# Performance work log

Hardware: AMD Instinct MI355X
Metric: run time of the kernel (lower is better)

## Reference

```python
import jax, jax.numpy as jnp
from jax import lax
import numpy as np

K, O, I, KS = 4, 128, 128, 5
B, H, W = 32, 64, 64
PAD = 2


def setup_inputs() -> dict:
    key = jax.random.key(0)
    ks = jax.random.split(key, 7)
    x = jax.random.normal(ks[0], (B, I, H, W), dtype=jnp.float32)
    weight = jax.random.normal(ks[1], (K, O, I, KS, KS), dtype=jnp.float32)  # matches torch.randn init
    bias = jax.random.normal(ks[2], (K, O), dtype=jnp.float32)
    # attention: 1x1 convs on a (B,C,1,1) pooled tensor == dense layers
    a1_w = jax.random.normal(ks[3], (I, I), dtype=jnp.float32) * (1.0 / np.sqrt(I))
    a1_b = jax.random.normal(ks[4], (I,), dtype=jnp.float32) * 0.01
    a2_w = jax.random.normal(ks[5], (K, I), dtype=jnp.float32) * (1.0 / np.sqrt(I))
    a2_b = jax.random.normal(ks[6], (K,), dtype=jnp.float32) * 0.01
    return {"x": x, "weight": weight, "bias": bias,
            "a1_w": a1_w, "a1_b": a1_b, "a2_w": a2_w, "a2_b": a2_b}


def reference(x, weight, bias, a1_w, a1_b, a2_w, a2_b):
    Bn = x.shape[0]
    Kn, On, In, kh, kw = weight.shape
    # attention branch: global avg pool -> 1x1 conv -> relu -> 1x1 conv -> softmax over K
    pooled = jnp.mean(x, axis=(2, 3))                       # (B, C)
    h = jax.nn.relu(pooled @ a1_w.T + a1_b)                 # (B, C)
    attn = jax.nn.softmax(h @ a2_w.T + a2_b, axis=1)        # (B, K)
    # K parallel convs fused as one conv with K*O output channels (same math)
    w = weight.reshape(Kn * On, In, kh, kw)
    out = lax.conv_general_dilated(
        x, w, window_strides=(1, 1), padding=((PAD, PAD), (PAD, PAD)),
        dimension_numbers=("NCHW", "OIHW", "NCHW"))        # (B, K*O, H, W)
    Ho, Wo = out.shape[2], out.shape[3]
    out = out.reshape(Bn, Kn, On, Ho, Wo) + bias[None, :, :, None, None]
    # per-sample softmax-weighted combination over the K branches
    return jnp.einsum("bk,bkohw->bohw", attn, out)
```

## Files before the change

kernel.cpp:

```cpp
#include <hip/hip_runtime.h>
#include <stdint.h>

#define BATCH 32
#define ICH 128
#define OCH 128
#define KBR 4
#define HH 64
#define WW 64
#define TAPS 25
#define XROWS 8
#define XCOLS 68
#define XCP 40
#define WROWP 40

typedef __bf16 bf16x8 __attribute__((ext_vector_type(8)));
typedef float f32x4 __attribute__((ext_vector_type(4)));

static __device__ __forceinline__ ushort f2bf(float f) {
    union { float f; uint32_t u; } v; v.f = f;
    uint32_t u = v.u;
    uint32_t r = (u + 0x7FFFu + ((u >> 16) & 1u)) >> 16;
    return (ushort)r;
}
static __device__ __forceinline__ float bf2f(ushort s) {
    union { uint32_t u; float f; } v; v.u = ((uint32_t)s) << 16;
    return v.f;
}

__global__ __launch_bounds__(256) void k_prep(const float* __restrict__ x,
                                              ushort* __restrict__ xT,
                                              float* __restrict__ partial) {
    int blk = blockIdx.x;
    int b = blk >> 6, y = blk & 63;
    __shared__ __align__(16) ushort tile[64][130];
    const float* src = x + ((size_t)b * ICH) * (HH * WW) + (size_t)y * WW;
    int tid = threadIdx.x;
#pragma unroll
    for (int j = 0; j < 8; ++j) {
        int e = (tid + 256 * j) * 4;
        int i = e >> 6, xc = e & 63;
        float4 v = *(const float4*)(src + (size_t)i * (HH * WW) + xc);
        tile[xc + 0][i] = f2bf(v.x);
        tile[xc + 1][i] = f2bf(v.y);
        tile[xc + 2][i] = f2bf(v.z);
        tile[xc + 3][i] = f2bf(v.w);
    }
    __syncthreads();
    uint* dst = (uint*)(xT + (((size_t)b * HH + y) * WW) * ICH);
#pragma unroll
    for (int j = 0; j < 16; ++j) {
        int p = tid + 256 * j;
        int xc = p >> 6, ih = (p & 63) * 2;
        uint v = (uint)tile[xc][ih] | ((uint)tile[xc][ih + 1] << 16);
        dst[p] = v;
    }
    if (tid < 128) {
        float s = 0.f;
        for (int xc = 0; xc < 64; ++xc) s += bf2f(tile[xc][tid]);
        partial[((size_t)b * HH + y) * ICH + tid] = s;
    }
}

__global__ __launch_bounds__(128) void k_attn(const float* __restrict__ partial,
                                              const float* __restrict__ a1_w,
                                              const float* __restrict__ a1_b,
                                              const float* __restrict__ a2_w,
                                              const float* __restrict__ a2_b,
                                              const float* __restrict__ bias,
                                              float* __restrict__ attn,
                                              float* __restrict__ bias_eff) {
    int b = blockIdx.x;
    int t = threadIdx.x;
    __shared__ float pl[128], hh[128], lg[4], at[4];
    {
        float s = 0.f;
        const float* p = partial + (size_t)b * 64 * 128 + t;
        for (int y = 0; y < 64; ++y) s += p[y * 128];
        pl[t] = s * (1.f / 4096.f);
    }
    __syncthreads();
    {
        float a = a1_b[t];
        const float* w1 = a1_w + t * 128;
        for (int i = 0; i < 128; ++i) a += pl[i] * w1[i];
        hh[t] = a > 0.f ? a : 0.f;
    }
    __syncthreads();
    if (t < 4) {
        float l = a2_b[t];
        const float* w2 = a2_w + t * 128;
        for (int i = 0; i < 128; ++i) l += hh[i] * w2[i];
        lg[t] = l;
    }
    __syncthreads();
    if (t == 0) {
        float m = fmaxf(fmaxf(lg[0], lg[1]), fmaxf(lg[2], lg[3]));
        float e0 = expf(lg[0] - m), e1 = expf(lg[1] - m);
        float e2 = expf(lg[2] - m), e3 = expf(lg[3] - m);
        float inv = 1.f / (e0 + e1 + e2 + e3);
        at[0] = e0 * inv; at[1] = e1 * inv; at[2] = e2 * inv; at[3] = e3 * inv;
        attn[b * 4 + 0] = at[0]; attn[b * 4 + 1] = at[1];
        attn[b * 4 + 2] = at[2]; attn[b * 4 + 3] = at[3];
    }
    __syncthreads();
    bias_eff[b * 128 + t] = at[0] * bias[0 * 128 + t] + at[1] * bias[1 * 128 + t] +
                            at[2] * bias[2 * 128 + t] + at[3] * bias[3 * 128 + t];
}

__global__ __launch_bounds__(256) void k_wcomb(const float* __restrict__ weight,
                                               const float* __restrict__ attn,
                                               ushort* __restrict__ Weff) {
    int blk = blockIdx.x;
    int b = blk >> 7, o = blk & 127;
    float a0 = attn[b * 4 + 0], a1 = attn[b * 4 + 1];
    float a2 = attn[b * 4 + 2], a3 = attn[b * 4 + 3];
    __shared__ float wt[3200];
    const float* w = weight + (size_t)o * 3200;
    for (int e = threadIdx.x; e < 3200; e += 256) {
        wt[e] = a0 * w[e] + a1 * w[409600 + e] + a2 * w[819200 + e] + a3 * w[1228800 + e];
    }
    __syncthreads();
    ushort* dst = Weff + ((size_t)(b * 128 + o)) * 3200;
    for (int f = threadIdx.x; f < 3200; f += 256) {
        int t = f >> 7, i = f & 127;
        dst[f] = f2bf(wt[i * 25 + t]);
    }
}

__global__ __launch_bounds__(512) void k_conv(const ushort* __restrict__ xT,
                                              const ushort* __restrict__ Weff,
                                              const float* __restrict__ bias_eff,
                                              float* __restrict__ out) {
    __shared__ __align__(16) ushort lx[XROWS * XCOLS * XCP];
    __shared__ __align__(16) ushort lw[2][128 * WROWP];

    int blk = blockIdx.x;
    int xcd = blk & 7, slot = blk >> 3;
    int b = xcd * 4 + (slot >> 4);
    int rg = slot & 15;
    int y0 = rg * 4;
    int tid = threadIdx.x;
    int lane = tid & 63, wid = tid >> 6;
    int wm = wid >> 2, wn = wid & 3;
    int row16 = lane & 15, kg = lane >> 4;

    f32x4 acc[4][4];
    f32x4 zero = {0.f, 0.f, 0.f, 0.f};
#pragma unroll
    for (int m = 0; m < 4; ++m)
#pragma unroll
        for (int n = 0; n < 4; ++n) acc[m][n] = zero;

    const ushort* xb = xT + ((size_t)b * HH * WW) * ICH;
    const ushort* wb = Weff + ((size_t)b * OCH) * 3200;

    int wo = tid >> 2, wpart = tid & 3;

    {
        for (int q = tid; q < XROWS * XCOLS * 4; q += 512) {
            int s = q / (XCOLS * 4);
            int rem = q - s * (XCOLS * 4);
            int c = rem >> 2, part = rem & 3;
            int gy = y0 - 2 + s, gx = c - 2;
            uint4 val = make_uint4(0u, 0u, 0u, 0u);
            if (gy >= 0 && gy < 64 && gx >= 0 && gx < 64)
                val = *(const uint4*)(xb + ((size_t)(gy * 64 + gx)) * ICH + 0 + part * 8);
            *(uint4*)(&lx[(s * XCOLS + c) * XCP + part * 8]) = val;
        }
        uint4 wv = *(const uint4*)(wb + ((size_t)wo * 25 + 0) * 128 + 0 + wpart * 8);
        *(uint4*)(&lw[0][wo * WROWP + wpart * 8]) = wv;
    }
    __syncthreads();

    for (int g = 0; g < 100; ++g) {
        int buf = g & 1;
        int t = g % 25;
        uint4 wv;
        bool have_next = (g + 1 < 100);
        if (have_next) {
            int gn = g + 1;
            int icn = (gn / 25) * 32, tn = gn % 25;
            wv = *(const uint4*)(wb + ((size_t)wo * 25 + tn) * 128 + icn + wpart * 8);
        }
        {
            int kh = t / 5, kw = t - kh * 5;
            bf16x8 af[4], bfr[4];
#pragma unroll
            for (int m = 0; m < 4; ++m) {
                int o = wm * 64 + m * 16 + row16;
                af[m] = *(const bf16x8*)(&lw[buf][o * WROWP + kg * 8]);
            }
#pragma unroll
            for (int n = 0; n < 4; ++n) {
                int px = wn * 64 + n * 16 + row16;
                int yl = px >> 6, xc = px & 63;
                int s = yl + kh, cc = xc + kw;
                bfr[n] = *(const bf16x8*)(&lx[(s * XCOLS + cc) * XCP + kg * 8]);
            }
#pragma unroll
            for (int m = 0; m < 4; ++m)
#pragma unroll
                for (int n = 0; n < 4; ++n)
                    acc[m][n] = __builtin_amdgcn_mfma_f32_16x16x32_bf16(af[m], bfr[n], acc[m][n], 0, 0, 0);
        }
        if (have_next) {
            *(uint4*)(&lw[buf ^ 1][wo * WROWP + wpart * 8]) = wv;
        }
        if (t == 24) {
            __syncthreads();
            if (g < 99) {
                int icn = ((g + 1) / 25) * 32;
                for (int q = tid; q < XROWS * XCOLS * 4; q += 512) {
                    int s = q / (XCOLS * 4);
                    int rem = q - s * (XCOLS * 4);
                    int c = rem >> 2, part = rem & 3;
                    int gy = y0 - 2 + s, gx = c - 2;
                    uint4 val = make_uint4(0u, 0u, 0u, 0u);
                    if (gy >= 0 && gy < 64 && gx >= 0 && gx < 64)
                        val = *(const uint4*)(xb + ((size_t)(gy * 64 + gx)) * ICH + icn + part * 8);
                    *(uint4*)(&lx[(s * XCOLS + c) * XCP + part * 8]) = val;
                }
            }
            __syncthreads();
        } else {
            __syncthreads();
        }
    }

    float* ob = out + ((size_t)b * OCH) * (HH * WW);
#pragma unroll
    for (int m = 0; m < 4; ++m) {
#pragma unroll
        for (int r = 0; r < 4; ++r) {
            int o = wm * 64 + m * 16 + kg * 4 + r;
            float be = bias_eff[b * 128 + o];
#pragma unroll
            for (int n = 0; n < 4; ++n) {
                int px = wn * 64 + n * 16 + row16;
                int y = y0 + (px >> 6), xc = px & 63;
                ob[((size_t)o * 64 + y) * 64 + xc] = acc[m][n][r] + be;
            }
        }
    }
}

extern "C" void kernel_launch(void* const* d_in, const int* in_sizes, int n_in,
                              void* d_out, int out_size, void* d_ws, size_t ws_size,
                              hipStream_t stream) {
    const float* x      = (const float*)d_in[0];
    const float* weight = (const float*)d_in[1];
    const float* bias   = (const float*)d_in[2];
    const float* a1_w   = (const float*)d_in[3];
    const float* a1_b   = (const float*)d_in[4];
    const float* a2_w   = (const float*)d_in[5];
    const float* a2_b   = (const float*)d_in[6];
    float* out = (float*)d_out;

    const size_t WS_REQUIRED = 60834304;
    if (ws_size < WS_REQUIRED) return;

    char* ws = (char*)d_ws;
    ushort* xT       = (ushort*)(ws);
    ushort* Weff     = (ushort*)(ws + 33554432);
    float*  partial  = (float*)(ws + 59768832);
    float*  attn     = (float*)(ws + 60817408);
    float*  bias_eff = (float*)(ws + 60817920);

    k_prep<<<dim3(BATCH * HH), dim3(256), 0, stream>>>(x, xT, partial);
    k_attn<<<dim3(BATCH), dim3(128), 0, stream>>>(partial, a1_w, a1_b, a2_w, a2_b, bias,
                                                  attn, bias_eff);
    k_wcomb<<<dim3(BATCH * OCH), dim3(256), 0, stream>>>(weight, attn, Weff);
    k_conv<<<dim3(BATCH * 16), dim3(512), 0, stream>>>(xT, Weff, bias_eff, out);
}
```

Measured before the change: 241.2 us.

## Halve conv block to 4 waves each covering all 128 outputs; pack prep transpose

The conv kernel now uses 256 threads (4 waves) instead of 512. Each wave owns one output row and all 128 output channels, with 8x4 MFMA tiles per wave, so the B (input) fragments are reused across twice as many A fragments. Launch bounds request 2 blocks per CU, and each thread now loads two weight vectors per step. The prep kernel transposes pairs of channels packed into 32-bit words, which avoids 16-bit LDS writes and repacking on readout. The trade-off is more accumulator registers per thread (128 floats), which risks occupancy pressure or spills, and fewer waves per block to hide latency.

Result: no change. 242.6 us (+0.6%).

```diff
diff --git a/kernel.cpp b/kernel.cpp
--- a/kernel.cpp
+++ b/kernel.cpp
@@ -32,31 +32,35 @@
                                               float* __restrict__ partial) {
     int blk = blockIdx.x;
     int b = blk >> 6, y = blk & 63;
-    __shared__ __align__(16) ushort tile[64][130];
+    __shared__ __align__(16) uint tile2[64][65];
     const float* src = x + ((size_t)b * ICH) * (HH * WW) + (size_t)y * WW;
     int tid = threadIdx.x;
 #pragma unroll
-    for (int j = 0; j < 8; ++j) {
-        int e = (tid + 256 * j) * 4;
-        int i = e >> 6, xc = e & 63;
-        float4 v = *(const float4*)(src + (size_t)i * (HH * WW) + xc);
-        tile[xc + 0][i] = f2bf(v.x);
-        tile[xc + 1][i] = f2bf(v.y);
-        tile[xc + 2][i] = f2bf(v.z);
-        tile[xc + 3][i] = f2bf(v.w);
+    for (int j = 0; j < 4; ++j) {
+        int p = tid + 256 * j;
+        int i2 = p >> 4, xc = (p & 15) * 4;
+        float4 v0 = *(const float4*)(src + (size_t)(2 * i2) * (HH * WW) + xc);
+        float4 v1 = *(const float4*)(src + (size_t)(2 * i2 + 1) * (HH * WW) + xc);
+        tile2[xc + 0][i2] = (uint)f2bf(v0.x) | ((uint)f2bf(v1.x) << 16);
+        tile2[xc + 1][i2] = (uint)f2bf(v0.y) | ((uint)f2bf(v1.y) << 16);
+        tile2[xc + 2][i2] = (uint)f2bf(v0.z) | ((uint)f2bf(v1.z) << 16);
+        tile2[xc + 3][i2] = (uint)f2bf(v0.w) | ((uint)f2bf(v1.w) << 16);
     }
     __syncthreads();
     uint* dst = (uint*)(xT + (((size_t)b * HH + y) * WW) * ICH);
 #pragma unroll
     for (int j = 0; j < 16; ++j) {
-        int p = tid + 256 * j;
-        int xc = p >> 6, ih = (p & 63) * 2;
-        uint v = (uint)tile[xc][ih] | ((uint)tile[xc][ih + 1] << 16);
-        dst[p] = v;
+        int p2 = tid + 256 * j;
+        int xc = p2 >> 6, i2 = p2 & 63;
+        dst[p2] = tile2[xc][i2];
     }
     if (tid < 128) {
+        int i2 = tid >> 1, half = tid & 1;
         float s = 0.f;
-        for (int xc = 0; xc < 64; ++xc) s += bf2f(tile[xc][tid]);
+        for (int xc = 0; xc < 64; ++xc) {
+            uint v = tile2[xc][i2];
+            s += bf2f((ushort)(half ? (v >> 16) : (v & 0xFFFFu)));
+        }
         partial[((size_t)b * HH + y) * ICH + tid] = s;
     }
 }
@@ -127,10 +131,10 @@
     }
 }
 
-__global__ __launch_bounds__(512) void k_conv(const ushort* __restrict__ xT,
-                                              const ushort* __restrict__ Weff,
-                                              const float* __restrict__ bias_eff,
-                                              float* __restrict__ out) {
+__global__ __launch_bounds__(256, 2) void k_conv(const ushort* __restrict__ xT,
+                                                 const ushort* __restrict__ Weff,
+                                                 const float* __restrict__ bias_eff,
+                                                 float* __restrict__ out) {
     __shared__ __align__(16) ushort lx[XROWS * XCOLS * XCP];
     __shared__ __align__(16) ushort lw[2][128 * WROWP];
 
@@ -140,24 +144,24 @@
     int rg = slot & 15;
     int y0 = rg * 4;
     int tid = threadIdx.x;
-    int lane = tid & 63, wid = tid >> 6;
-    int wm = wid >> 2, wn = wid & 3;
+    int lane = tid & 63, wn = tid >> 6;
     int row16 = lane & 15, kg = lane >> 4;
 
-    f32x4 acc[4][4];
+    f32x4 acc[8][4];
     f32x4 zero = {0.f, 0.f, 0.f, 0.f};
 #pragma unroll
-    for (int m = 0; m < 4; ++m)
+    for (int m = 0; m < 8; ++m)
 #pragma unroll
         for (int n = 0; n < 4; ++n) acc[m][n] = zero;
 
     const ushort* xb = xT + ((size_t)b * HH * WW) * ICH;
     const ushort* wb = Weff + ((size_t)b * OCH) * 3200;
 
-    int wo = tid >> 2, wpart = tid & 3;
+    int wo0 = tid >> 2, wp0 = tid & 3;
+    int wo1 = (tid + 256) >> 2, wp1 = tid & 3;
 
     {
-        for (int q = tid; q < XROWS * XCOLS * 4; q += 512) {
+        for (int q = tid; q < XROWS * XCOLS * 4; q += 256) {
             int s = q / (XCOLS * 4);
             int rem = q - s * (XCOLS * 4);
             int c = rem >> 2, part = rem & 3;
@@ -167,50 +171,53 @@
                 val = *(const uint4*)(xb + ((size_t)(gy * 64 + gx)) * ICH + 0 + part * 8);
             *(uint4*)(&lx[(s * XCOLS + c) * XCP + part * 8]) = val;
         }
-        uint4 wv = *(const uint4*)(wb + ((size_t)wo * 25 + 0) * 128 + 0 + wpart * 8);
-        *(uint4*)(&lw[0][wo * WROWP + wpart * 8]) = wv;
+        uint4 w0 = *(const uint4*)(wb + ((size_t)wo0 * 25 + 0) * 128 + 0 + wp0 * 8);
+        uint4 w1 = *(const uint4*)(wb + ((size_t)wo1 * 25 + 0) * 128 + 0 + wp1 * 8);
+        *(uint4*)(&lw[0][wo0 * WROWP + wp0 * 8]) = w0;
+        *(uint4*)(&lw[0][wo1 * WROWP + wp1 * 8]) = w1;
     }
     __syncthreads();
 
     for (int g = 0; g < 100; ++g) {
         int buf = g & 1;
         int t = g % 25;
-        uint4 wv;
+        uint4 wv0, wv1;
         bool have_next = (g + 1 < 100);
         if (have_next) {
             int gn = g + 1;
             int icn = (gn / 25) * 32, tn = gn % 25;
-            wv = *(const uint4*)(wb + ((size_t)wo * 25 + tn) * 128 + icn + wpart * 8);
+            wv0 = *(const uint4*)(wb + ((size_t)wo0 * 25 + tn) * 128 + icn + wp0 * 8);
+            wv1 = *(const uint4*)(wb + ((size_t)wo1 * 25 + tn) * 128 + icn + wp1 * 8);
         }
         {
             int kh = t / 5, kw = t - kh * 5;
-            bf16x8 af[4], bfr[4];
-#pragma unroll
-            for (int m = 0; m < 4; ++m) {
-                int o = wm * 64 + m * 16 + row16;
+            int s = wn + kh;
+            bf16x8 af[8], bfr[4];
+#pragma unroll
+            for (int n = 0; n < 4; ++n) {
+                int cc = n * 16 + row16 + kw;
+                bfr[n] = *(const bf16x8*)(&lx[(s * XCOLS + cc) * XCP + kg * 8]);
+            }
+#pragma unroll
+            for (int m = 0; m < 8; ++m) {
+                int o = m * 16 + row16;
                 af[m] = *(const bf16x8*)(&lw[buf][o * WROWP + kg * 8]);
             }
 #pragma unroll
-            for (int n = 0; n < 4; ++n) {
-                int px = wn * 64 + n * 16 + row16;
-                int yl = px >> 6, xc = px & 63;
-                int s = yl + kh, cc = xc + kw;
-                bfr[n] = *(const bf16x8*)(&lx[(s * XCOLS + cc) * XCP + kg * 8]);
-            }
-#pragma unroll
-            for (int m = 0; m < 4; ++m)
+            for (int m = 0; m < 8; ++m)
 #pragma unroll
                 for (int n = 0; n < 4; ++n)
                     acc[m][n] = __builtin_amdgcn_mfma_f32_16x16x32_bf16(af[m], bfr[n], acc[m][n], 0, 0, 0);
         }
         if (have_next) {
-            *(uint4*)(&lw[buf ^ 1][wo * WROWP + wpart * 8]) = wv;
+            *(uint4*)(&lw[buf ^ 1][wo0 * WROWP + wp0 * 8]) = wv0;
+            *(uint4*)(&lw[buf ^ 1][wo1 * WROWP + wp1 * 8]) = wv1;
         }
         if (t == 24) {
             __syncthreads();
             if (g < 99) {
                 int icn = ((g + 1) / 25) * 32;
-                for (int q = tid; q < XROWS * XCOLS * 4; q += 512) {
+                for (int q = tid; q < XROWS * XCOLS * 4; q += 256) {
                     int s = q / (XCOLS * 4);
                     int rem = q - s * (XCOLS * 4);
                     int c = rem >> 2, part = rem & 3;
@@ -228,16 +235,16 @@
     }
 
     float* ob = out + ((size_t)b * OCH) * (HH * WW);
-#pragma unroll
-    for (int m = 0; m < 4; ++m) {
+    int y = y0 + wn;
+#pragma unroll
+    for (int m = 0; m < 8; ++m) {
 #pragma unroll
         for (int r = 0; r < 4; ++r) {
-            int o = wm * 64 + m * 16 + kg * 4 + r;
+            int o = m * 16 + kg * 4 + r;
             float be = bias_eff[b * 128 + o];
 #pragma unroll
             for (int n = 0; n < 4; ++n) {
-                int px = wn * 64 + n * 16 + row16;
-                int y = y0 + (px >> 6), xc = px & 63;
+                int xc = n * 16 + row16;
                 ob[((size_t)o * 64 + y) * 64 + xc] = acc[m][n][r] + be;
             }
         }
@@ -270,5 +277,5 @@
     k_attn<<<dim3(BATCH), dim3(128), 0, stream>>>(partial, a1_w, a1_b, a2_w, a2_b, bias,
                                                   attn, bias_eff);
     k_wcomb<<<dim3(BATCH * OCH), dim3(256), 0, stream>>>(weight, attn, Weff);
-    k_conv<<<dim3(BATCH * 16), dim3(512), 0, stream>>>(xT, Weff, bias_eff, out);
-}
+    k_conv<<<dim3(BATCH * 16), dim3(256), 0, stream>>>(xT, Weff, bias_eff, out);
+}
```
